# Optimization experiments

Measured on AMD Instinct MI355X. Metric: run time of the kernel, lower is better.

## Reference

```python
import jax, jax.numpy as jnp
import numpy as np

B, S, D_IN, D_HEAD = 4, 4096, 1024, 64

def setup_inputs() -> dict:
    key = jax.random.key(0)
    k1, k2, k3, k4 = jax.random.split(key, 4)
    scale = 0.02
    return {
        "input_vectors": jax.random.normal(k1, (B, S, D_IN), dtype=jnp.float32),
        "Wq": jax.random.normal(k2, (D_IN, D_HEAD), dtype=jnp.float32) * scale,
        "Wk": jax.random.normal(k3, (D_IN, D_HEAD), dtype=jnp.float32) * scale,
        "Wv": jax.random.normal(k4, (D_IN, D_HEAD), dtype=jnp.float32) * scale,
    }

def reference(input_vectors, Wq, Wk, Wv):
    # QKV projections (Linear with no bias): [B,S,d_in] @ [d_in,d_head]
    q = input_vectors @ Wq  # [B,S,H]
    k = input_vectors @ Wk
    v = input_vectors @ Wv
    n = input_vectors.shape[1]
    # causal attention scores: [B,S,S]
    scores = jnp.einsum('bqh,bkh->bqk', q, k)
    causal = jnp.tril(jnp.ones((n, n), dtype=bool))  # True = keep
    scores = jnp.where(causal, scores, -jnp.inf)
    scale = k.shape[-1] ** -0.5
    attn = jax.nn.softmax(scores * scale, axis=-1)
    return jnp.einsum('bqk,bkh->bqh', attn, v)
```

## Files before the change

kernel.cpp:

```cpp
#include <hip/hip_runtime.h>
#include <stdint.h>

#define SEQ   4096
#define DHEAD 64
#define DIN   1024

typedef __attribute__((ext_vector_type(8))) short bf16x8;
typedef __attribute__((ext_vector_type(4))) float floatx4;

#if __has_builtin(__builtin_amdgcn_exp2f)
#define EXP2(x) __builtin_amdgcn_exp2f(x)
#else
#define EXP2(x) exp2f(x)
#endif

__device__ __forceinline__ unsigned short f2bf(float f) {
    union { float f; unsigned int u; } v; v.f = f;
    unsigned int u = v.u + 0x7fffu + ((v.u >> 16) & 1u);
    return (unsigned short)(u >> 16);
}

__device__ __forceinline__ void g2l16(const void* g, const void* l) {
    __builtin_amdgcn_global_load_lds(
        (__attribute__((address_space(1))) unsigned int*)(uintptr_t)g,
        (__attribute__((address_space(3))) unsigned int*)(unsigned int)(uintptr_t)l,
        16, 0, 0);
}

__global__ void wt_prep(const float* __restrict__ Wq, const float* __restrict__ Wk,
                        const float* __restrict__ Wv, unsigned short* __restrict__ WT) {
    int idx = blockIdx.x * 256 + threadIdx.x;
    int k   = idx & 1023;
    int n   = (idx >> 10) & 63;
    int mat = idx >> 16;
    const float* W = (mat == 0) ? Wq : ((mat == 1) ? Wk : Wv);
    WT[idx] = f2bf(W[k * 64 + n]);
}

#define QSCALE 0.18033688011112042f
__launch_bounds__(256, 4)
__global__ void proj_qkv(const float* __restrict__ X, const unsigned short* __restrict__ WT,
                         unsigned short* __restrict__ qb, unsigned short* __restrict__ kb,
                         unsigned short* __restrict__ vb) {
    __shared__ __align__(16) float          Xl[16 * 64];
    __shared__ __align__(16) unsigned short Wl[192 * 64];
    const int tid = threadIdx.x;
    const int wave = tid >> 6, lane = tid & 63;
    const int quad = lane >> 4, l16 = lane & 15;
    const int row0 = blockIdx.x * 16;
    const int m = l16;

    floatx4 acc[3];
#pragma unroll
    for (int i = 0; i < 3; i++) acc[i] = (floatx4){0.f, 0.f, 0.f, 0.f};

    for (int kc = 0; kc < 16; kc++) {
        const int k0 = kc * 64;
        __syncthreads();
        {
            int u = tid;
            int r = u >> 4, cp = u & 15, c = cp ^ (r & 15);
            g2l16(X + (size_t)(row0 + r) * DIN + k0 + c * 4, Xl + u * 4);
        }
#pragma unroll
        for (int i = 0; i < 6; i++) {
            int u = (wave * 6 + i) * 64 + lane;
            int r = u >> 3, cp = u & 7, c = cp ^ (r & 7);
            g2l16(WT + (size_t)r * 1024 + k0 + c * 8, Wl + u * 8);
        }
        __syncthreads();
        bf16x8 af[2];
#pragma unroll
        for (int ks = 0; ks < 2; ks++) {
            floatx4 x0 = *(const floatx4*)&Xl[m * 64 + ((ks * 8 + quad * 2 + 0) ^ m) * 4];
            floatx4 x1 = *(const floatx4*)&Xl[m * 64 + ((ks * 8 + quad * 2 + 1) ^ m) * 4];
#pragma unroll
            for (int j = 0; j < 4; j++) {
                af[ks][j]     = (short)f2bf(x0[j]);
                af[ks][j + 4] = (short)f2bf(x1[j]);
            }
        }
#pragma unroll
        for (int i = 0; i < 3; i++) {
            const int nrow = (wave * 3 + i) * 16 + l16;
#pragma unroll
            for (int ks = 0; ks < 2; ks++) {
                const int c = ks * 4 + quad;
                bf16x8 bfrag = *(const bf16x8*)&Wl[nrow * 64 + (c ^ (nrow & 7)) * 8];
                acc[i] = __builtin_amdgcn_mfma_f32_16x16x32_bf16(af[ks], bfrag, acc[i], 0, 0, 0);
            }
        }
    }
#pragma unroll
    for (int i = 0; i < 3; i++) {
        const int nt = wave * 3 + i;
        const int mat = nt >> 2;
        const int col = (nt & 3) * 16 + l16;
#pragma unroll
        for (int r = 0; r < 4; r++) {
            const int orow = row0 + quad * 4 + r;
            float v = acc[i][r];
            if (mat == 0) {
                qb[(size_t)orow * 64 + col] = f2bf(v * QSCALE);
            } else if (mat == 1) {
                kb[(size_t)orow * 64 + col] = f2bf(v);
            } else {
                int b = orow >> 12, s = orow & 4095;
                vb[((size_t)b * 64 + col) * SEQ + s] = f2bf(v);
            }
        }
    }
}

__launch_bounds__(256, 4)
__global__ void attn(const unsigned short* __restrict__ qb, const unsigned short* __restrict__ kb,
                     const unsigned short* __restrict__ vb, float* __restrict__ opart,
                     float* __restrict__ lpart) {
    __shared__ __align__(16) unsigned short Kl[128 * 64];
    __shared__ __align__(16) unsigned short Vl[64 * 128];
    __shared__ __align__(16) unsigned short Pl[4][16 * 72];
    __shared__ float Ll[2][16][16];
    float* Ol = (float*)Kl;

    const int bid = blockIdx.x;
    const int hkb   = bid & 1;
    const int batch = (bid >> 1) & 3;
    const int qidx  = bid >> 3;
    const int h = (qidx >> 5) & 1;
    const int f = (qidx & 31) | ((qidx >> 6) << 5);
    const int qt = h ? 127 - f : f;
    const int q0 = qt * 32;
    const int tid = threadIdx.x;
    const int wave = tid >> 6, lane = tid & 63;
    const int quad = lane >> 4, l16 = lane & 15;
    const int strip = wave & 1, kh = wave >> 1;

    const int Tfull = (q0 + 32 + 127) >> 7;
    const int T0 = (Tfull + 1) >> 1;
    const int ktlo = hkb ? T0 : 0;
    const int kthi = hkb ? Tfull : T0;

    const unsigned short* qrow = qb + (size_t)(batch * SEQ + q0 + strip * 16 + l16) * 64;
    bf16x8 qa[2];
    qa[0] = *(const bf16x8*)(qrow + quad * 8);
    qa[1] = *(const bf16x8*)(qrow + 32 + quad * 8);

    floatx4 o[4];
#pragma unroll
    for (int i = 0; i < 4; i++) o[i] = (floatx4){0.f, 0.f, 0.f, 0.f};
    float lrow[4] = {0.f, 0.f, 0.f, 0.f};

    const unsigned short* kbase = kb + (size_t)batch * SEQ * 64;
    const unsigned short* vbase = vb + (size_t)batch * 64 * SEQ;

    for (int kt = ktlo; kt < kthi; kt++) {
        const int k0 = kt * 128;
        __syncthreads();
#pragma unroll
        for (int i = 0; i < 4; i++) {
            int u = (wave * 4 + i) * 64 + lane;
            int r = u >> 3, cp = u & 7, c = cp ^ (r & 7);
            g2l16(kbase + (size_t)(k0 + r) * 64 + c * 8, Kl + u * 8);
        }
#pragma unroll
        for (int i = 0; i < 4; i++) {
            int u = (wave * 4 + i) * 64 + lane;
            int d = u >> 4, cp = u & 15, c = cp ^ (d & 15);
            g2l16(vbase + (size_t)d * SEQ + k0 + c * 8, Vl + u * 8);
        }
        __syncthreads();

        floatx4 sc[4];
#pragma unroll
        for (int nt = 0; nt < 4; nt++) {
            sc[nt] = (floatx4){0.f, 0.f, 0.f, 0.f};
            const int key = kh * 64 + nt * 16 + l16;
#pragma unroll
            for (int ks = 0; ks < 2; ks++) {
                const int c = ks * 4 + quad;
                bf16x8 bk = *(const bf16x8*)&Kl[key * 64 + (c ^ (key & 7)) * 8];
                sc[nt] = __builtin_amdgcn_mfma_f32_16x16x32_bf16(qa[ks], bk, sc[nt], 0, 0, 0);
            }
        }
        if (kt == Tfull - 1) {
#pragma unroll
            for (int nt = 0; nt < 4; nt++) {
                const int col = k0 + kh * 64 + nt * 16 + l16;
#pragma unroll
                for (int r = 0; r < 4; r++) {
                    const int rowg = q0 + strip * 16 + quad * 4 + r;
                    if (col > rowg) sc[nt][r] = -1e30f;
                }
            }
        }
        unsigned short* P = &Pl[wave][0];
#pragma unroll
        for (int r = 0; r < 4; r++) {
#pragma unroll
            for (int nt = 0; nt < 4; nt++) {
                float p = EXP2(sc[nt][r]);
                lrow[r] += p;
                P[(quad * 4 + r) * 72 + nt * 16 + l16] = f2bf(p);
            }
        }
        bf16x8 pa[2];
        pa[0] = *(const bf16x8*)&P[l16 * 72 + quad * 8];
        pa[1] = *(const bf16x8*)&P[l16 * 72 + 32 + quad * 8];
#pragma unroll
        for (int nt = 0; nt < 4; nt++) {
            const int d = nt * 16 + l16;
#pragma unroll
            for (int ks = 0; ks < 2; ks++) {
                const int c = kh * 8 + ks * 4 + quad;
                bf16x8 bv = *(const bf16x8*)&Vl[d * 128 + (c ^ (d & 15)) * 8];
                o[nt] = __builtin_amdgcn_mfma_f32_16x16x32_bf16(pa[ks], bv, o[nt], 0, 0, 0);
            }
        }
    }

    __syncthreads();
    if (kh == 1) {
#pragma unroll
        for (int nt = 0; nt < 4; nt++)
#pragma unroll
            for (int r = 0; r < 4; r++)
                Ol[strip * 1024 + (quad * 4 + r) * 64 + nt * 16 + l16] = o[nt][r];
#pragma unroll
        for (int r = 0; r < 4; r++) Ll[strip][quad * 4 + r][l16] = lrow[r];
    }
    __syncthreads();
    if (kh == 0) {
#pragma unroll
        for (int nt = 0; nt < 4; nt++)
#pragma unroll
            for (int r = 0; r < 4; r++)
                o[nt][r] += Ol[strip * 1024 + (quad * 4 + r) * 64 + nt * 16 + l16];
        float* ob = opart + (size_t)hkb * (4 * SEQ * 64)
                  + (size_t)(batch * SEQ + q0 + strip * 16) * 64;
        float* lb = lpart + (size_t)hkb * (4 * SEQ)
                  + (size_t)(batch * SEQ + q0 + strip * 16);
#pragma unroll
        for (int r = 0; r < 4; r++) {
            float l = lrow[r] + Ll[strip][quad * 4 + r][l16];
            l += __shfl_xor(l, 1);
            l += __shfl_xor(l, 2);
            l += __shfl_xor(l, 4);
            l += __shfl_xor(l, 8);
#pragma unroll
            for (int nt = 0; nt < 4; nt++)
                ob[(quad * 4 + r) * 64 + nt * 16 + l16] = o[nt][r];
            if (l16 == 0) lb[quad * 4 + r] = l;
        }
    }
}

__global__ void merge(const float* __restrict__ opart, const float* __restrict__ lpart,
                      float* __restrict__ out) {
    int idx = blockIdx.x * 256 + threadIdx.x;
    int row = idx >> 4, c4 = idx & 15;
    floatx4 a = *(const floatx4*)(opart + (size_t)row * 64 + c4 * 4);
    floatx4 b = *(const floatx4*)(opart + (size_t)(4 * SEQ * 64) + (size_t)row * 64 + c4 * 4);
    float inv = 1.f / (lpart[row] + lpart[4 * SEQ + row]);
    floatx4 r = (a + b) * inv;
    *(floatx4*)(out + (size_t)row * 64 + c4 * 4) = r;
}

extern "C" void kernel_launch(void* const* d_in, const int* in_sizes, int n_in,
                              void* d_out, int out_size, void* d_ws, size_t ws_size,
                              hipStream_t stream) {
    const float* X  = (const float*)d_in[0];
    const float* Wq = (const float*)d_in[1];
    const float* Wk = (const float*)d_in[2];
    const float* Wv = (const float*)d_in[3];
    float* out = (float*)d_out;
    char* ws = (char*)d_ws;
    unsigned short* WT = (unsigned short*)ws;
    unsigned short* qb = (unsigned short*)(ws + 393216);
    unsigned short* kb = (unsigned short*)(ws + 393216 + 2097152);
    unsigned short* vb = (unsigned short*)(ws + 393216 + 2 * 2097152);
    float* opart = (float*)(ws + 393216 + 3 * 2097152);
    float* lpart = (float*)(ws + 393216 + 3 * 2097152 + 8388608);

    hipLaunchKernelGGL(wt_prep,  dim3(768),  dim3(256), 0, stream, Wq, Wk, Wv, WT);
    hipLaunchKernelGGL(proj_qkv, dim3(1024), dim3(256), 0, stream, X, WT, qb, kb, vb);
    hipLaunchKernelGGL(attn,     dim3(1024), dim3(256), 0, stream, qb, kb, vb, opart, lpart);
    hipLaunchKernelGGL(merge,    dim3(1024), dim3(256), 0, stream, opart, lpart, out);
}
```

Baseline: 152.0 us.

## Register-prefetch pipelining, 4-way balanced split-K attention with bf16 partials

Both the projection and attention kernels swap direct global-to-LDS loads for register prefetching, so the next tile's global loads overlap the current tile's MFMA work. Attention now uses 64-row query tiles with 64-key tiles and a 4-way split over key tiles, with a balanced block-to-rank mapping. This removes the in-block cross-wave LDS reduction of the previous two-half key split. Partial outputs are stored as bf16 and merged across four splits, which halves partial traffic but adds rounding error and more merge reads.

```diff
diff --git a/kernel.cpp b/kernel.cpp
--- a/kernel.cpp
+++ b/kernel.cpp
@@ -7,6 +7,7 @@
 
 typedef __attribute__((ext_vector_type(8))) short bf16x8;
 typedef __attribute__((ext_vector_type(4))) float floatx4;
+typedef __attribute__((ext_vector_type(4))) unsigned short ushortx4;
 
 #if __has_builtin(__builtin_amdgcn_exp2f)
 #define EXP2(x) __builtin_amdgcn_exp2f(x)
@@ -19,12 +20,9 @@
     unsigned int u = v.u + 0x7fffu + ((v.u >> 16) & 1u);
     return (unsigned short)(u >> 16);
 }
-
-__device__ __forceinline__ void g2l16(const void* g, const void* l) {
-    __builtin_amdgcn_global_load_lds(
-        (__attribute__((address_space(1))) unsigned int*)(uintptr_t)g,
-        (__attribute__((address_space(3))) unsigned int*)(unsigned int)(uintptr_t)l,
-        16, 0, 0);
+__device__ __forceinline__ float bf2f(unsigned short h) {
+    union { unsigned int u; float f; } v; v.u = ((unsigned int)h) << 16;
+    return v.f;
 }
 
 __global__ void wt_prep(const float* __restrict__ Wq, const float* __restrict__ Wk,
@@ -54,21 +52,35 @@
 #pragma unroll
     for (int i = 0; i < 3; i++) acc[i] = (floatx4){0.f, 0.f, 0.f, 0.f};
 
+    floatx4 xpre;
+    floatx4 wpre[6];
+
+    const int xu = tid, xr = xu >> 4, xc = (xu & 15) ^ (xr & 15);
+    int wu[6], wr[6], wc[6];
+#pragma unroll
+    for (int i = 0; i < 6; i++) {
+        wu[i] = (wave * 6 + i) * 64 + lane;
+        wr[i] = wu[i] >> 3;
+        wc[i] = (wu[i] & 7) ^ (wr[i] & 7);
+    }
+
+    auto issue = [&](int k0) {
+        xpre = *(const floatx4*)(X + (size_t)(row0 + xr) * DIN + k0 + xc * 4);
+#pragma unroll
+        for (int i = 0; i < 6; i++)
+            wpre[i] = *(const floatx4*)(WT + (size_t)wr[i] * 1024 + k0 + wc[i] * 8);
+    };
+
+    issue(0);
     for (int kc = 0; kc < 16; kc++) {
-        const int k0 = kc * 64;
-        __syncthreads();
-        {
-            int u = tid;
-            int r = u >> 4, cp = u & 15, c = cp ^ (r & 15);
-            g2l16(X + (size_t)(row0 + r) * DIN + k0 + c * 4, Xl + u * 4);
-        }
-#pragma unroll
-        for (int i = 0; i < 6; i++) {
-            int u = (wave * 6 + i) * 64 + lane;
-            int r = u >> 3, cp = u & 7, c = cp ^ (r & 7);
-            g2l16(WT + (size_t)r * 1024 + k0 + c * 8, Wl + u * 8);
-        }
-        __syncthreads();
+        __syncthreads();
+        *(floatx4*)&Xl[xu * 4] = xpre;
+#pragma unroll
+        for (int i = 0; i < 6; i++)
+            *(floatx4*)&Wl[wu[i] * 8] = wpre[i];
+        __syncthreads();
+        if (kc < 15) issue((kc + 1) * 64);
+
         bf16x8 af[2];
 #pragma unroll
         for (int ks = 0; ks < 2; ks++) {
@@ -114,33 +126,29 @@
 
 __launch_bounds__(256, 4)
 __global__ void attn(const unsigned short* __restrict__ qb, const unsigned short* __restrict__ kb,
-                     const unsigned short* __restrict__ vb, float* __restrict__ opart,
+                     const unsigned short* __restrict__ vb, unsigned short* __restrict__ opart,
                      float* __restrict__ lpart) {
-    __shared__ __align__(16) unsigned short Kl[128 * 64];
-    __shared__ __align__(16) unsigned short Vl[64 * 128];
+    __shared__ __align__(16) unsigned short Kl[64 * 64];
+    __shared__ __align__(16) unsigned short Vl[64 * 64];
     __shared__ __align__(16) unsigned short Pl[4][16 * 72];
-    __shared__ float Ll[2][16][16];
-    float* Ol = (float*)Kl;
 
     const int bid = blockIdx.x;
-    const int hkb   = bid & 1;
-    const int batch = (bid >> 1) & 3;
-    const int qidx  = bid >> 3;
-    const int h = (qidx >> 5) & 1;
-    const int f = (qidx & 31) | ((qidx >> 6) << 5);
-    const int qt = h ? 127 - f : f;
-    const int q0 = qt * 32;
+    const int batch = bid & 3;
+    const int mm = bid >> 2;
+    const int idx = mm & 63, g = mm >> 6;
+    const int rank = (g == 0) ? (255 - idx) : (g == 1) ? (128 + idx)
+                   : (g == 2) ? (127 - idx) : idx;
+    const int qt = rank >> 2, s = rank & 3;
+    const int q0 = qt * 64;
+    const int T = qt + 1;
+    const int ktlo = (T * s) >> 2;
+    const int kthi = (T * (s + 1)) >> 2;
+
     const int tid = threadIdx.x;
     const int wave = tid >> 6, lane = tid & 63;
     const int quad = lane >> 4, l16 = lane & 15;
-    const int strip = wave & 1, kh = wave >> 1;
-
-    const int Tfull = (q0 + 32 + 127) >> 7;
-    const int T0 = (Tfull + 1) >> 1;
-    const int ktlo = hkb ? T0 : 0;
-    const int kthi = hkb ? Tfull : T0;
-
-    const unsigned short* qrow = qb + (size_t)(batch * SEQ + q0 + strip * 16 + l16) * 64;
+
+    const unsigned short* qrow = qb + (size_t)(batch * SEQ + q0 + wave * 16 + l16) * 64;
     bf16x8 qa[2];
     qa[0] = *(const bf16x8*)(qrow + quad * 8);
     qa[1] = *(const bf16x8*)(qrow + 32 + quad * 8);
@@ -153,28 +161,38 @@
     const unsigned short* kbase = kb + (size_t)batch * SEQ * 64;
     const unsigned short* vbase = vb + (size_t)batch * 64 * SEQ;
 
+    int ku[2], kr[2], kc_[2], vu[2], vd[2], vc[2];
+#pragma unroll
+    for (int i = 0; i < 2; i++) {
+        ku[i] = i * 256 + tid; kr[i] = ku[i] >> 3; kc_[i] = (ku[i] & 7) ^ (kr[i] & 7);
+        vu[i] = i * 256 + tid; vd[i] = vu[i] >> 3; vc[i] = (vu[i] & 7) ^ (vd[i] & 7);
+    }
+    floatx4 kpre[2], vpre[2];
+    auto issue = [&](int k0) {
+#pragma unroll
+        for (int i = 0; i < 2; i++)
+            kpre[i] = *(const floatx4*)(kbase + (size_t)(k0 + kr[i]) * 64 + kc_[i] * 8);
+#pragma unroll
+        for (int i = 0; i < 2; i++)
+            vpre[i] = *(const floatx4*)(vbase + (size_t)vd[i] * SEQ + k0 + vc[i] * 8);
+    };
+
+    if (ktlo < kthi) issue(ktlo * 64);
     for (int kt = ktlo; kt < kthi; kt++) {
-        const int k0 = kt * 128;
-        __syncthreads();
-#pragma unroll
-        for (int i = 0; i < 4; i++) {
-            int u = (wave * 4 + i) * 64 + lane;
-            int r = u >> 3, cp = u & 7, c = cp ^ (r & 7);
-            g2l16(kbase + (size_t)(k0 + r) * 64 + c * 8, Kl + u * 8);
-        }
-#pragma unroll
-        for (int i = 0; i < 4; i++) {
-            int u = (wave * 4 + i) * 64 + lane;
-            int d = u >> 4, cp = u & 15, c = cp ^ (d & 15);
-            g2l16(vbase + (size_t)d * SEQ + k0 + c * 8, Vl + u * 8);
-        }
-        __syncthreads();
-
+        __syncthreads();
+#pragma unroll
+        for (int i = 0; i < 2; i++) *(floatx4*)&Kl[ku[i] * 8] = kpre[i];
+#pragma unroll
+        for (int i = 0; i < 2; i++) *(floatx4*)&Vl[vu[i] * 8] = vpre[i];
+        __syncthreads();
+        if (kt + 1 < kthi) issue((kt + 1) * 64);
+
+        const int k0 = kt * 64;
         floatx4 sc[4];
 #pragma unroll
         for (int nt = 0; nt < 4; nt++) {
             sc[nt] = (floatx4){0.f, 0.f, 0.f, 0.f};
-            const int key = kh * 64 + nt * 16 + l16;
+            const int key = nt * 16 + l16;
 #pragma unroll
             for (int ks = 0; ks < 2; ks++) {
                 const int c = ks * 4 + quad;
@@ -182,13 +200,13 @@
                 sc[nt] = __builtin_amdgcn_mfma_f32_16x16x32_bf16(qa[ks], bk, sc[nt], 0, 0, 0);
             }
         }
-        if (kt == Tfull - 1) {
+        if (kt == T - 1) {
 #pragma unroll
             for (int nt = 0; nt < 4; nt++) {
-                const int col = k0 + kh * 64 + nt * 16 + l16;
+                const int col = k0 + nt * 16 + l16;
 #pragma unroll
                 for (int r = 0; r < 4; r++) {
-                    const int rowg = q0 + strip * 16 + quad * 4 + r;
+                    const int rowg = q0 + wave * 16 + quad * 4 + r;
                     if (col > rowg) sc[nt][r] = -1e30f;
                 }
             }
@@ -211,58 +229,46 @@
             const int d = nt * 16 + l16;
 #pragma unroll
             for (int ks = 0; ks < 2; ks++) {
-                const int c = kh * 8 + ks * 4 + quad;
-                bf16x8 bv = *(const bf16x8*)&Vl[d * 128 + (c ^ (d & 15)) * 8];
+                const int c = ks * 4 + quad;
+                bf16x8 bv = *(const bf16x8*)&Vl[d * 64 + (c ^ (d & 7)) * 8];
                 o[nt] = __builtin_amdgcn_mfma_f32_16x16x32_bf16(pa[ks], bv, o[nt], 0, 0, 0);
             }
         }
     }
 
-    __syncthreads();
-    if (kh == 1) {
+    unsigned short* ob = opart + (size_t)s * (4 * SEQ * 64)
+                       + (size_t)(batch * SEQ + q0 + wave * 16) * 64;
+    float* lb = lpart + (size_t)s * (4 * SEQ) + (size_t)(batch * SEQ + q0 + wave * 16);
+#pragma unroll
+    for (int r = 0; r < 4; r++) {
+        float l = lrow[r];
+        l += __shfl_xor(l, 1);
+        l += __shfl_xor(l, 2);
+        l += __shfl_xor(l, 4);
+        l += __shfl_xor(l, 8);
 #pragma unroll
         for (int nt = 0; nt < 4; nt++)
-#pragma unroll
-            for (int r = 0; r < 4; r++)
-                Ol[strip * 1024 + (quad * 4 + r) * 64 + nt * 16 + l16] = o[nt][r];
-#pragma unroll
-        for (int r = 0; r < 4; r++) Ll[strip][quad * 4 + r][l16] = lrow[r];
-    }
-    __syncthreads();
-    if (kh == 0) {
-#pragma unroll
-        for (int nt = 0; nt < 4; nt++)
-#pragma unroll
-            for (int r = 0; r < 4; r++)
-                o[nt][r] += Ol[strip * 1024 + (quad * 4 + r) * 64 + nt * 16 + l16];
-        float* ob = opart + (size_t)hkb * (4 * SEQ * 64)
-                  + (size_t)(batch * SEQ + q0 + strip * 16) * 64;
-        float* lb = lpart + (size_t)hkb * (4 * SEQ)
-                  + (size_t)(batch * SEQ + q0 + strip * 16);
-#pragma unroll
-        for (int r = 0; r < 4; r++) {
-            float l = lrow[r] + Ll[strip][quad * 4 + r][l16];
-            l += __shfl_xor(l, 1);
-            l += __shfl_xor(l, 2);
-            l += __shfl_xor(l, 4);
-            l += __shfl_xor(l, 8);
-#pragma unroll
-            for (int nt = 0; nt < 4; nt++)
-                ob[(quad * 4 + r) * 64 + nt * 16 + l16] = o[nt][r];
-            if (l16 == 0) lb[quad * 4 + r] = l;
-        }
-    }
-}
-
-__global__ void merge(const float* __restrict__ opart, const float* __restrict__ lpart,
+            ob[(quad * 4 + r) * 64 + nt * 16 + l16] = f2bf(o[nt][r]);
+        if (l16 == 0) lb[quad * 4 + r] = l;
+    }
+}
+
+__global__ void merge(const unsigned short* __restrict__ opart, const float* __restrict__ lpart,
                       float* __restrict__ out) {
     int idx = blockIdx.x * 256 + threadIdx.x;
     int row = idx >> 4, c4 = idx & 15;
-    floatx4 a = *(const floatx4*)(opart + (size_t)row * 64 + c4 * 4);
-    floatx4 b = *(const floatx4*)(opart + (size_t)(4 * SEQ * 64) + (size_t)row * 64 + c4 * 4);
-    float inv = 1.f / (lpart[row] + lpart[4 * SEQ + row]);
-    floatx4 r = (a + b) * inv;
-    *(floatx4*)(out + (size_t)row * 64 + c4 * 4) = r;
+    float l = lpart[row] + lpart[4 * SEQ + row] + lpart[8 * SEQ + row] + lpart[12 * SEQ + row];
+    float inv = 1.f / l;
+    floatx4 acc = (floatx4){0.f, 0.f, 0.f, 0.f};
+#pragma unroll
+    for (int s = 0; s < 4; s++) {
+        ushortx4 u = *(const ushortx4*)(opart + (size_t)s * (4 * SEQ * 64)
+                                        + (size_t)row * 64 + c4 * 4);
+#pragma unroll
+        for (int j = 0; j < 4; j++) acc[j] += bf2f(u[j]);
+    }
+    acc *= inv;
+    *(floatx4*)(out + (size_t)row * 64 + c4 * 4) = acc;
 }
 
 extern "C" void kernel_launch(void* const* d_in, const int* in_sizes, int n_in,
@@ -278,7 +284,7 @@
     unsigned short* qb = (unsigned short*)(ws + 393216);
     unsigned short* kb = (unsigned short*)(ws + 393216 + 2097152);
     unsigned short* vb = (unsigned short*)(ws + 393216 + 2 * 2097152);
-    float* opart = (float*)(ws + 393216 + 3 * 2097152);
+    unsigned short* opart = (unsigned short*)(ws + 393216 + 3 * 2097152);
     float* lpart = (float*)(ws + 393216 + 3 * 2097152 + 8388608);
 
     hipLaunchKernelGGL(wt_prep,  dim3(768),  dim3(256), 0, stream, Wq, Wk, Wv, WT);
```

Result: faster. 144.9 us (-4.7%).
